# Kernel tuning notes

Measured on AMD Instinct MI355X. Metric: run time of the kernel, lower is better.

The kernel has to match this reference:

```python
import jax, jax.numpy as jnp
import numpy as np

NUM_HEADS = 4
HEAD_DIM = 64  # out_dim // num_heads
NEG_INF = -9e15


def setup_inputs() -> dict:
    key = jax.random.key(0)
    k1, k2, k3, k4 = jax.random.split(key, 4)
    b, n, in_dim, out_dim = 8, 1024, 256, 256
    x = jax.random.normal(k1, (b, n, in_dim), dtype=jnp.float32)
    adj = jax.random.uniform(k2, (b, n, n), dtype=jnp.float32)
    # linear_proj weight, stored as [in_dim, out_dim] (xavier-ish scale)
    Wp = jax.random.normal(k3, (in_dim, out_dim), dtype=jnp.float32) * (1.0 / np.sqrt(in_dim))
    # scoring_fn weight for concat([left(64), right(64), adj(1)]) -> 1
    Ws = jax.random.normal(k4, (2 * HEAD_DIM + 1,), dtype=jnp.float32) * (1.0 / np.sqrt(HEAD_DIM))
    bias = jnp.zeros((out_dim,), dtype=jnp.float32)
    return {"x": x, "adj": adj, "Wp": Wp, "Ws": Ws, "bias": bias}


def reference(x, adj, Wp, Ws, bias):
    b, n, _ = x.shape
    H, hd = NUM_HEADS, HEAD_DIM
    # manifold_in = Euclidean -> logmap0 is identity; dropout is eval (p=0)
    proj = (x @ Wp).reshape(b, n, H, hd)  # [b,n,H,hd]
    # scoring_fn(cat[left, right, adj]) decomposed: score = left.w_l + right.w_r + adj*w_a
    w_l, w_r, w_a = Ws[:hd], Ws[hd:2 * hd], Ws[2 * hd]
    s_l = jnp.einsum('bnhd,d->bnh', proj, w_l)  # dest-node term
    s_r = jnp.einsum('bmhd,d->bmh', proj, w_r)  # src-node term
    score = s_l[:, :, None, :] + s_r[:, None, :, :] + (adj * w_a)[..., None]  # [b,n,n,H]
    score = jax.nn.leaky_relu(score, 0.2)
    # local_agg: mask out non-edges (adj <= 1e-5) by adding -9e15
    pad = (adj <= 1e-5).astype(score.dtype)
    score = score + (NEG_INF * pad)[..., None]
    att = jax.nn.softmax(score, axis=2)  # softmax over source nodes m
    # msg[b,i,h,d] = sum_m att[b,i,m,h] * proj[b,m,h,d]
    msg = jnp.einsum('bimh,bmhd->bihd', att, proj).reshape(b, n, H * hd)
    # in_dim == out_dim -> no skip_proj; Euclidean expmap0/transp0/expmap: out = x + msg + bias
    out = x + msg + bias
    out = jax.nn.leaky_relu(out, 0.5)  # act = LeakyReLU(0.5)
    return out, adj
```

## Files before the change

kernel.cpp:

```cpp
#include <hip/hip_runtime.h>

#define NHEADS 4
#define HDIM   64
#define BATCH  8
#define SEQ    1024
#define CH     256
#define LOG2E  1.4426950408889634f
#define MC     128
#define NC     (SEQ / MC)
#define LDP    132

typedef float  f32x4  __attribute__((ext_vector_type(4)));
typedef __bf16 bf16x8 __attribute__((ext_vector_type(8)));
typedef short  s16x8  __attribute__((ext_vector_type(8)));
union FU { s16x8 s; bf16x8 b; };

__device__ inline unsigned short f2bf(float f) {
    unsigned u = __float_as_uint(f);
    return (unsigned short)((u + 0x7fffu + ((u >> 16) & 1u)) >> 16);
}
__device__ inline float4 nt_load4(const float* p) {
    f32x4 v = __builtin_nontemporal_load(reinterpret_cast<const f32x4*>(p));
    return make_float4(v.x, v.y, v.z, v.w);
}
__device__ inline void nt_store4(float* p, float4 v) {
    f32x4 u = {v.x, v.y, v.z, v.w};
    __builtin_nontemporal_store(u, reinterpret_cast<f32x4*>(p));
}


__global__ __launch_bounds__(256) void wpt_cast(const float* __restrict__ Wp,
                                                unsigned short* __restrict__ WpT) {
    __shared__ float T[32][33];
    const int t = threadIdx.x;
    const int kt = blockIdx.x * 32, ct = blockIdx.y * 32;
    const int r = t >> 3, c4 = (t & 7) * 4;
    float4 v = *reinterpret_cast<const float4*>(&Wp[(size_t)(kt + r) * CH + ct + c4]);
    T[r][c4 + 0] = v.x; T[r][c4 + 1] = v.y; T[r][c4 + 2] = v.z; T[r][c4 + 3] = v.w;
    __syncthreads();
    unsigned p0 = (unsigned)f2bf(T[c4 + 0][r]) | ((unsigned)f2bf(T[c4 + 1][r]) << 16);
    unsigned p1 = (unsigned)f2bf(T[c4 + 2][r]) | ((unsigned)f2bf(T[c4 + 3][r]) << 16);
    uint2 o = make_uint2(p0, p1);
    *reinterpret_cast<uint2*>(&WpT[(size_t)(ct + r) * CH + kt + c4]) = o;
}

__global__ __launch_bounds__(256, 2) void proj_fused(const float* __restrict__ x,
                                                     const unsigned short* __restrict__ WpT,
                                                     const float* __restrict__ Ws,
                                                     unsigned short* __restrict__ projT,
                                                     float* __restrict__ sl,
                                                     float* __restrict__ sr) {
    const int t = threadIdx.x, w = t >> 6, l = t & 63, il = l & 15, g = l >> 4;
    const int row0 = blockIdx.x * 16;
    const int b = row0 >> 10, n0 = row0 & 1023;

    const unsigned short* Ap = WpT + (size_t)(w * 64 + il) * CH + g * 8;
    const float*          Bp = x + (size_t)(row0 + il) * CH + g * 8;

    float4 xv[8][2];
#pragma unroll
    for (int kt = 0; kt < 8; ++kt) {
        xv[kt][0] = *reinterpret_cast<const float4*>(Bp + kt * 32);
        xv[kt][1] = *reinterpret_cast<const float4*>(Bp + kt * 32 + 4);
    }

    f32x4 acc[4] = {};
#pragma unroll
    for (int kt = 0; kt < 8; ++kt) {
        FU a[4], bb;
#pragma unroll
        for (int ai = 0; ai < 4; ++ai)
            a[ai].s = *reinterpret_cast<const s16x8*>(Ap + (size_t)ai * 16 * CH + kt * 32);
        bb.b[0] = (__bf16)xv[kt][0].x; bb.b[1] = (__bf16)xv[kt][0].y;
        bb.b[2] = (__bf16)xv[kt][0].z; bb.b[3] = (__bf16)xv[kt][0].w;
        bb.b[4] = (__bf16)xv[kt][1].x; bb.b[5] = (__bf16)xv[kt][1].y;
        bb.b[6] = (__bf16)xv[kt][1].z; bb.b[7] = (__bf16)xv[kt][1].w;
#pragma unroll
        for (int ai = 0; ai < 4; ++ai)
            acc[ai] = __builtin_amdgcn_mfma_f32_16x16x32_bf16(a[ai].b, bb.b, acc[ai], 0, 0, 0);
    }

    unsigned short* pS = projT + (((size_t)(b * NHEADS + w)) << 16)
                       + (size_t)(n0 >> 4) * 1024 + (il >> 3) * 128 + (il & 7);
#pragma unroll
    for (int ai = 0; ai < 4; ++ai)
#pragma unroll
        for (int q = 0; q < 4; ++q)
            pS[ai * 256 + (g * 4 + q) * 8] = f2bf(acc[ai][q]);

    float pl = 0.f, pr = 0.f;
#pragma unroll
    for (int ai = 0; ai < 4; ++ai) {
        float4 wlv = *reinterpret_cast<const float4*>(&Ws[ai * 16 + g * 4]);
        float4 wrv = *reinterpret_cast<const float4*>(&Ws[HDIM + ai * 16 + g * 4]);
        pl += acc[ai][0] * wlv.x + acc[ai][1] * wlv.y + acc[ai][2] * wlv.z + acc[ai][3] * wlv.w;
        pr += acc[ai][0] * wrv.x + acc[ai][1] * wrv.y + acc[ai][2] * wrv.z + acc[ai][3] * wrv.w;
    }
    pl += __shfl_xor(pl, 16); pl += __shfl_xor(pl, 32);
    pr += __shfl_xor(pr, 16); pr += __shfl_xor(pr, 32);
    if (l < 16) {
        sl[(size_t)(b * NHEADS + w) * SEQ + n0 + il] = pl * LOG2E;
        sr[(size_t)(b * NHEADS + w) * SEQ + n0 + il] = pr * LOG2E;
    }
}

template <bool FUSE_ADJ>
__global__ __launch_bounds__(256, 2) void attn12(const float* __restrict__ x,
                                                 const float* __restrict__ adj,
                                                 const unsigned short* __restrict__ projT,
                                                 const float* __restrict__ sl,
                                                 const float* __restrict__ sr,
                                                 const float* __restrict__ Ws,
                                                 const float* __restrict__ bias,
                                                 float* __restrict__ out,
                                                 float* __restrict__ out_adj) {
    __shared__ __align__(16) float abuf[2][16][LDP];

    const int t = threadIdx.x;
    const int h = t >> 6, l = t & 63, il = l & 15, g = l >> 4;
    const int b  = blockIdx.x & 7;
    const int i0 = (blockIdx.x >> 3) * 16;
    const float wa2 = Ws[2 * HDIM] * LOG2E;

    const int str = t >> 4;
    const int stc = (t & 15) * 4;
    const size_t astg = ((size_t)(b * SEQ + i0 + str)) * SEQ + stc;

    const float sl_i = sl[(size_t)(b * NHEADS + h) * SEQ + i0 + il];
    const float* srp = sr + (size_t)(b * NHEADS + h) * SEQ;
    const unsigned short* pTsw = projT + (((size_t)(b * NHEADS + h)) << 16)
                               + (g >> 1) * 1024 + (g & 1) * 128 + il * 8;

    FU ones;
#pragma unroll
    for (int j = 0; j < 8; ++j) ones.s[j] = (short)0x3F80;

    f32x4 acc[4] = {};
    f32x4 dacc = {};

    float4 c00 = nt_load4(adj + astg);
    float4 c01 = nt_load4(adj + astg + 64);
    float4 cur0 = nt_load4(adj + astg + MC);
    float4 cur1 = nt_load4(adj + astg + MC + 64);
    if (FUSE_ADJ) {
        nt_store4(out_adj + astg, c00);
        nt_store4(out_adj + astg + 64, c01);
    }
    *reinterpret_cast<float4*>(&abuf[0][str][stc])      = c00;
    *reinterpret_cast<float4*>(&abuf[0][str][stc + 64]) = c01;
    __syncthreads();

    for (int c = 0; c < NC; ++c) {
        float4 nx0 = {}, nx1 = {};
        if (c + 2 < NC) {
            nx0 = nt_load4(adj + astg + (size_t)(c + 2) * MC);
            nx1 = nt_load4(adj + astg + (size_t)(c + 2) * MC + 64);
        }
        const float* aT = &abuf[c & 1][il][0];
        const int mt = c * MC;

        float4 av[4][2], sv4[4][2];
        FU B[4][4];
#pragma unroll
        for (int kq = 0; kq < 4; ++kq) {
            const int mk = kq * 32 + g * 8;
            av[kq][0]  = *reinterpret_cast<const float4*>(aT + mk);
            av[kq][1]  = *reinterpret_cast<const float4*>(aT + mk + 4);
            sv4[kq][0] = *reinterpret_cast<const float4*>(srp + mt + mk);
            sv4[kq][1] = *reinterpret_cast<const float4*>(srp + mt + mk + 4);
        }
#pragma unroll
        for (int kq = 0; kq < 4; ++kq) {
#pragma unroll
            for (int bj = 0; bj < 4; ++bj)
                B[kq][bj].s = *reinterpret_cast<const s16x8*>(
                    pTsw + c * 8192 + kq * 2048 + bj * 256);
        }

        FU af[4];
#pragma unroll
        for (int kq = 0; kq < 4; ++kq) {
            float aj[8] = {av[kq][0].x, av[kq][0].y, av[kq][0].z, av[kq][0].w,
                           av[kq][1].x, av[kq][1].y, av[kq][1].z, av[kq][1].w};
            float sv[8] = {sv4[kq][0].x, sv4[kq][0].y, sv4[kq][0].z, sv4[kq][0].w,
                           sv4[kq][1].x, sv4[kq][1].y, sv4[kq][1].z, sv4[kq][1].w};
#pragma unroll
            for (int j = 0; j < 8; ++j) {
                float s = fmaf(aj[j], wa2, sl_i + sv[j]);
                s = __builtin_amdgcn_fmed3f(s, 0.2f * s, 86.5617f);
                float e = (aj[j] <= 1e-5f) ? 0.f : __builtin_amdgcn_exp2f(s);
                af[kq].b[j] = (__bf16)e;
            }
        }

#pragma unroll
        for (int kq = 0; kq < 4; ++kq) {
            acc[0] = __builtin_amdgcn_mfma_f32_16x16x32_bf16(af[kq].b, B[kq][0].b, acc[0], 0, 0, 0);
            acc[1] = __builtin_amdgcn_mfma_f32_16x16x32_bf16(af[kq].b, B[kq][1].b, acc[1], 0, 0, 0);
            acc[2] = __builtin_amdgcn_mfma_f32_16x16x32_bf16(af[kq].b, B[kq][2].b, acc[2], 0, 0, 0);
            acc[3] = __builtin_amdgcn_mfma_f32_16x16x32_bf16(af[kq].b, B[kq][3].b, acc[3], 0, 0, 0);
            dacc   = __builtin_amdgcn_mfma_f32_16x16x32_bf16(af[kq].b, ones.b,   dacc,   0, 0, 0);
        }

        if (c + 1 < NC) {
            if (FUSE_ADJ) {
                nt_store4(out_adj + astg + (size_t)(c + 1) * MC, cur0);
                nt_store4(out_adj + astg + (size_t)(c + 1) * MC + 64, cur1);
            }
            *reinterpret_cast<float4*>(&abuf[(c + 1) & 1][str][stc])      = cur0;
            *reinterpret_cast<float4*>(&abuf[(c + 1) & 1][str][stc + 64]) = cur1;
        }
        __syncthreads();
        cur0 = nx0; cur1 = nx1;
    }

    const float* bb = bias + h * HDIM;
#pragma unroll
    for (int q = 0; q < 4; ++q) {
        const float inv = 1.f / dacc[q];
        const size_t ob = ((size_t)(b * SEQ + i0 + g * 4 + q)) * CH + h * HDIM + il;
#pragma unroll
        for (int bj = 0; bj < 4; ++bj) {
            float v = fmaf(acc[bj][q], inv, x[ob + bj * 16] + bb[bj * 16 + il]);
            v = fmaxf(v, 0.5f * v);
            __builtin_nontemporal_store(v, out + ob + bj * 16);
        }
    }
}

__global__ void adjcopy(const float* __restrict__ adj, float* __restrict__ dst, int n4) {
    int idx = blockIdx.x * blockDim.x + threadIdx.x;
    int stride = gridDim.x * blockDim.x;
    const float4* s = reinterpret_cast<const float4*>(adj);
    float4* d = reinterpret_cast<float4*>(dst);
    for (int i = idx; i < n4; i += stride) d[i] = s[i];
}

extern "C" void kernel_launch(void* const* d_in, const int* in_sizes, int n_in,
                              void* d_out, int out_size, void* d_ws, size_t ws_size,
                              hipStream_t stream) {
    const float* x    = (const float*)d_in[0];
    const float* adj  = (const float*)d_in[1];
    const float* Wp   = (const float*)d_in[2];
    const float* Ws   = (const float*)d_in[3];
    const float* bias = (const float*)d_in[4];
    float* out     = (float*)d_out;
    float* out_adj = out + (size_t)BATCH * SEQ * CH;

    const size_t nProj = (size_t)BATCH * SEQ * CH;
    const size_t nSc   = (size_t)BATCH * NHEADS * SEQ;
    const size_t need  = CH * CH * 2 + nProj * 2 + 2 * nSc * 4;
    const bool use_ws  = (ws_size >= need);
    char* scratch = use_ws ? (char*)d_ws : (char*)out_adj;
    unsigned short* WpT   = (unsigned short*)scratch;
    unsigned short* projT = (unsigned short*)(scratch + (size_t)CH * CH * 2);
    float*          sl    = (float*)(scratch + (size_t)CH * CH * 2 + nProj * 2);
    float*          sr    = sl + nSc;

    wpt_cast<<<dim3(8, 8), 256, 0, stream>>>(Wp, WpT);
    proj_fused<<<dim3(512), 256, 0, stream>>>(x, WpT, Ws, projT, sl, sr);
    if (use_ws) {
        attn12<true><<<dim3(512), 256, 0, stream>>>(
            x, adj, projT, sl, sr, Ws, bias, out, out_adj);
    } else {
        attn12<false><<<dim3(512), 256, 0, stream>>>(
            x, adj, projT, sl, sr, Ws, bias, out, out_adj);
        adjcopy<<<2048, 256, 0, stream>>>(adj, out_adj, (BATCH * SEQ * SEQ) / 4);
    }
}
```

Baseline: 53.92 us.

## Split source-node range across two wave groups per block with LDS reduction

The attention kernel now runs 512 threads per block, with two groups of four waves that each handle half of the source-node range (512 columns), so each wave loops over 4 chunks instead of 8. Partial message accumulators and softmax denominators from the second half are written to shared memory, then summed by the first half before the epilogue. This shortens each wave's serial loop and raises the number of in-flight adj loads per block. In exchange it doubles shared memory for the adjacency staging, adds a block-wide reduction, and may reduce how many blocks fit per CU.

Result: faster. 51.26 us, median of 2 (-4.9%).

```diff
diff --git a/kernel.cpp b/kernel.cpp
--- a/kernel.cpp
+++ b/kernel.cpp
@@ -7,7 +7,6 @@
 #define CH     256
 #define LOG2E  1.4426950408889634f
 #define MC     128
-#define NC     (SEQ / MC)
 #define LDP    132
 
 typedef float  f32x4  __attribute__((ext_vector_type(4)));
@@ -105,7 +104,7 @@
 }
 
 template <bool FUSE_ADJ>
-__global__ __launch_bounds__(256, 2) void attn12(const float* __restrict__ x,
+__global__ __launch_bounds__(512, 2) void attn13(const float* __restrict__ x,
                                                  const float* __restrict__ adj,
                                                  const unsigned short* __restrict__ projT,
                                                  const float* __restrict__ sl,
@@ -114,21 +113,24 @@
                                                  const float* __restrict__ bias,
                                                  float* __restrict__ out,
                                                  float* __restrict__ out_adj) {
-    __shared__ __align__(16) float abuf[2][16][LDP];
+    __shared__ __align__(16) float abuf[2][2][16][LDP];
 
     const int t = threadIdx.x;
-    const int h = t >> 6, l = t & 63, il = l & 15, g = l >> 4;
+    const int w = t >> 6, l = t & 63, il = l & 15, g = l >> 4;
+    const int h = w & 3, mh = w >> 2;
     const int b  = blockIdx.x & 7;
     const int i0 = (blockIdx.x >> 3) * 16;
     const float wa2 = Ws[2 * HDIM] * LOG2E;
 
-    const int str = t >> 4;
+    const int sh = t >> 8;
+    const int str = (t >> 4) & 15;
     const int stc = (t & 15) * 4;
-    const size_t astg = ((size_t)(b * SEQ + i0 + str)) * SEQ + stc;
+    const size_t astg = ((size_t)(b * SEQ + i0 + str)) * SEQ + sh * 512 + stc;
 
     const float sl_i = sl[(size_t)(b * NHEADS + h) * SEQ + i0 + il];
-    const float* srp = sr + (size_t)(b * NHEADS + h) * SEQ;
+    const float* srp = sr + (size_t)(b * NHEADS + h) * SEQ + mh * 512;
     const unsigned short* pTsw = projT + (((size_t)(b * NHEADS + h)) << 16)
+                               + (size_t)mh * 32768
                                + (g >> 1) * 1024 + (g & 1) * 128 + il * 8;
 
     FU ones;
@@ -146,17 +148,17 @@
         nt_store4(out_adj + astg, c00);
         nt_store4(out_adj + astg + 64, c01);
     }
-    *reinterpret_cast<float4*>(&abuf[0][str][stc])      = c00;
-    *reinterpret_cast<float4*>(&abuf[0][str][stc + 64]) = c01;
+    *reinterpret_cast<float4*>(&abuf[0][sh][str][stc])      = c00;
+    *reinterpret_cast<float4*>(&abuf[0][sh][str][stc + 64]) = c01;
     __syncthreads();
 
-    for (int c = 0; c < NC; ++c) {
+    for (int c = 0; c < 4; ++c) {
         float4 nx0 = {}, nx1 = {};
-        if (c + 2 < NC) {
+        if (c + 2 < 4) {
             nx0 = nt_load4(adj + astg + (size_t)(c + 2) * MC);
             nx1 = nt_load4(adj + astg + (size_t)(c + 2) * MC + 64);
         }
-        const float* aT = &abuf[c & 1][il][0];
+        const float* aT = &abuf[c & 1][mh][il][0];
         const int mt = c * MC;
 
         float4 av[4][2], sv4[4][2];
@@ -202,28 +204,46 @@
             dacc   = __builtin_amdgcn_mfma_f32_16x16x32_bf16(af[kq].b, ones.b,   dacc,   0, 0, 0);
         }
 
-        if (c + 1 < NC) {
+        if (c + 1 < 4) {
             if (FUSE_ADJ) {
                 nt_store4(out_adj + astg + (size_t)(c + 1) * MC, cur0);
                 nt_store4(out_adj + astg + (size_t)(c + 1) * MC + 64, cur1);
             }
-            *reinterpret_cast<float4*>(&abuf[(c + 1) & 1][str][stc])      = cur0;
-            *reinterpret_cast<float4*>(&abuf[(c + 1) & 1][str][stc + 64]) = cur1;
+            *reinterpret_cast<float4*>(&abuf[(c + 1) & 1][sh][str][stc])      = cur0;
+            *reinterpret_cast<float4*>(&abuf[(c + 1) & 1][sh][str][stc + 64]) = cur1;
         }
         __syncthreads();
         cur0 = nx0; cur1 = nx1;
     }
 
-    const float* bb = bias + h * HDIM;
-#pragma unroll
-    for (int q = 0; q < 4; ++q) {
-        const float inv = 1.f / dacc[q];
-        const size_t ob = ((size_t)(b * SEQ + i0 + g * 4 + q)) * CH + h * HDIM + il;
-#pragma unroll
-        for (int bj = 0; bj < 4; ++bj) {
-            float v = fmaf(acc[bj][q], inv, x[ob + bj * 16] + bb[bj * 16 + il]);
-            v = fmaxf(v, 0.5f * v);
-            __builtin_nontemporal_store(v, out + ob + bj * 16);
+    float (*part)[16][68] = reinterpret_cast<float (*)[16][68]>(&abuf[0][0][0][0]);
+    if (mh == 1) {
+#pragma unroll
+        for (int bj = 0; bj < 4; ++bj)
+#pragma unroll
+            for (int q = 0; q < 4; ++q)
+                part[h][g * 4 + q][bj * 16 + il] = acc[bj][q];
+        if (il == 0) {
+#pragma unroll
+            for (int q = 0; q < 4; ++q) part[h][g * 4 + q][64] = dacc[q];
+        }
+    }
+    __syncthreads();
+    if (mh == 0) {
+        const float* bb = bias + h * HDIM;
+#pragma unroll
+        for (int q = 0; q < 4; ++q) {
+            const int row = g * 4 + q;
+            const float den = dacc[q] + part[h][row][64];
+            const float inv = 1.f / den;
+            const size_t ob = ((size_t)(b * SEQ + i0 + row)) * CH + h * HDIM + il;
+#pragma unroll
+            for (int bj = 0; bj < 4; ++bj) {
+                float m = acc[bj][q] + part[h][row][bj * 16 + il];
+                float v = fmaf(m, inv, x[ob + bj * 16] + bb[bj * 16 + il]);
+                v = fmaxf(v, 0.5f * v);
+                __builtin_nontemporal_store(v, out + ob + bj * 16);
+            }
         }
     }
 }
@@ -260,10 +280,10 @@
     wpt_cast<<<dim3(8, 8), 256, 0, stream>>>(Wp, WpT);
     proj_fused<<<dim3(512), 256, 0, stream>>>(x, WpT, Ws, projT, sl, sr);
     if (use_ws) {
-        attn12<true><<<dim3(512), 256, 0, stream>>>(
+        attn13<true><<<dim3(512), 512, 0, stream>>>(
             x, adj, projT, sl, sr, Ws, bias, out, out_adj);
     } else {
-        attn12<false><<<dim3(512), 256, 0, stream>>>(
+        attn13<false><<<dim3(512), 512, 0, stream>>>(
             x, adj, projT, sl, sr, Ws, bias, out, out_adj);
         adjcopy<<<2048, 256, 0, stream>>>(adj, out_adj, (BATCH * SEQ * SEQ) / 4);
     }
```

## Prefetch projT fragments one chunk ahead and stage sr scores in LDS

Applied to the files above, without the earlier changes.

The attention kernel now double-buffers the bf16 projT B fragments in registers, loading the next chunk's fragments while the current chunk's exponentials and MFMAs run. The per-head sr scores are copied once into shared memory instead of being re-read from global each chunk. The barrier becomes an inline asm waitcnt+s_barrier and the chunk loop is fully unrolled. These are meant to hide global load latency, at the cost of more VGPRs (two sets of 16 fragments), which risks spills or lower occupancy under launch_bounds(256,2), plus 16KB more LDS per block.

After: 52.93 us. About the same (-1.8%).

```diff
diff --git a/kernel.cpp b/kernel.cpp
--- a/kernel.cpp
+++ b/kernel.cpp
@@ -14,6 +14,8 @@
 typedef __bf16 bf16x8 __attribute__((ext_vector_type(8)));
 typedef short  s16x8  __attribute__((ext_vector_type(8)));
 union FU { s16x8 s; bf16x8 b; };
+
+#define BAR() asm volatile("s_waitcnt lgkmcnt(0)\n\ts_barrier" ::: "memory")
 
 __device__ inline unsigned short f2bf(float f) {
     unsigned u = __float_as_uint(f);
@@ -105,7 +107,7 @@
 }
 
 template <bool FUSE_ADJ>
-__global__ __launch_bounds__(256, 2) void attn12(const float* __restrict__ x,
+__global__ __launch_bounds__(256, 2) void attn14(const float* __restrict__ x,
                                                  const float* __restrict__ adj,
                                                  const unsigned short* __restrict__ projT,
                                                  const float* __restrict__ sl,
@@ -115,6 +117,7 @@
                                                  float* __restrict__ out,
                                                  float* __restrict__ out_adj) {
     __shared__ __align__(16) float abuf[2][16][LDP];
+    __shared__ __align__(16) float srl[NHEADS][SEQ];
 
     const int t = threadIdx.x;
     const int h = t >> 6, l = t & 63, il = l & 15, g = l >> 4;
@@ -127,7 +130,7 @@
     const size_t astg = ((size_t)(b * SEQ + i0 + str)) * SEQ + stc;
 
     const float sl_i = sl[(size_t)(b * NHEADS + h) * SEQ + i0 + il];
-    const float* srp = sr + (size_t)(b * NHEADS + h) * SEQ;
+    const float* srg = sr + (size_t)(b * NHEADS + h) * SEQ;
     const unsigned short* pTsw = projT + (((size_t)(b * NHEADS + h)) << 16)
                                + (g >> 1) * 1024 + (g & 1) * 128 + il * 8;
 
@@ -138,6 +141,11 @@
     f32x4 acc[4] = {};
     f32x4 dacc = {};
 
+#pragma unroll
+    for (int k = 0; k < 4; ++k) {
+        float4 sv = *reinterpret_cast<const float4*>(srg + l * 16 + k * 4);
+        *reinterpret_cast<float4*>(&srl[h][l * 16 + k * 4]) = sv;
+    }
     float4 c00 = nt_load4(adj + astg);
     float4 c01 = nt_load4(adj + astg + 64);
     float4 cur0 = nt_load4(adj + astg + MC);
@@ -148,35 +156,41 @@
     }
     *reinterpret_cast<float4*>(&abuf[0][str][stc])      = c00;
     *reinterpret_cast<float4*>(&abuf[0][str][stc + 64]) = c01;
+    FU Bb[2][4][4];
+#pragma unroll
+    for (int kq = 0; kq < 4; ++kq)
+#pragma unroll
+        for (int bj = 0; bj < 4; ++bj)
+            Bb[0][kq][bj].s = *reinterpret_cast<const s16x8*>(pTsw + kq * 2048 + bj * 256);
     __syncthreads();
 
+#pragma unroll
     for (int c = 0; c < NC; ++c) {
+        const int cb = c & 1, nb = cb ^ 1;
         float4 nx0 = {}, nx1 = {};
         if (c + 2 < NC) {
             nx0 = nt_load4(adj + astg + (size_t)(c + 2) * MC);
             nx1 = nt_load4(adj + astg + (size_t)(c + 2) * MC + 64);
         }
-        const float* aT = &abuf[c & 1][il][0];
-        const int mt = c * MC;
-
+        if (c + 1 < NC) {
+#pragma unroll
+            for (int kq = 0; kq < 4; ++kq)
+#pragma unroll
+                for (int bj = 0; bj < 4; ++bj)
+                    Bb[nb][kq][bj].s = *reinterpret_cast<const s16x8*>(
+                        pTsw + (c + 1) * 8192 + kq * 2048 + bj * 256);
+        }
+        const float* aT = &abuf[cb][il][0];
+        const float* sT = &srl[h][c * MC];
         float4 av[4][2], sv4[4][2];
-        FU B[4][4];
 #pragma unroll
         for (int kq = 0; kq < 4; ++kq) {
             const int mk = kq * 32 + g * 8;
             av[kq][0]  = *reinterpret_cast<const float4*>(aT + mk);
             av[kq][1]  = *reinterpret_cast<const float4*>(aT + mk + 4);
-            sv4[kq][0] = *reinterpret_cast<const float4*>(srp + mt + mk);
-            sv4[kq][1] = *reinterpret_cast<const float4*>(srp + mt + mk + 4);
-        }
-#pragma unroll
-        for (int kq = 0; kq < 4; ++kq) {
-#pragma unroll
-            for (int bj = 0; bj < 4; ++bj)
-                B[kq][bj].s = *reinterpret_cast<const s16x8*>(
-                    pTsw + c * 8192 + kq * 2048 + bj * 256);
-        }
-
+            sv4[kq][0] = *reinterpret_cast<const float4*>(sT + mk);
+            sv4[kq][1] = *reinterpret_cast<const float4*>(sT + mk + 4);
+        }
         FU af[4];
 #pragma unroll
         for (int kq = 0; kq < 4; ++kq) {
@@ -192,25 +206,23 @@
                 af[kq].b[j] = (__bf16)e;
             }
         }
-
 #pragma unroll
         for (int kq = 0; kq < 4; ++kq) {
-            acc[0] = __builtin_amdgcn_mfma_f32_16x16x32_bf16(af[kq].b, B[kq][0].b, acc[0], 0, 0, 0);
-            acc[1] = __builtin_amdgcn_mfma_f32_16x16x32_bf16(af[kq].b, B[kq][1].b, acc[1], 0, 0, 0);
-            acc[2] = __builtin_amdgcn_mfma_f32_16x16x32_bf16(af[kq].b, B[kq][2].b, acc[2], 0, 0, 0);
-            acc[3] = __builtin_amdgcn_mfma_f32_16x16x32_bf16(af[kq].b, B[kq][3].b, acc[3], 0, 0, 0);
-            dacc   = __builtin_amdgcn_mfma_f32_16x16x32_bf16(af[kq].b, ones.b,   dacc,   0, 0, 0);
-        }
-
+            acc[0] = __builtin_amdgcn_mfma_f32_16x16x32_bf16(af[kq].b, Bb[cb][kq][0].b, acc[0], 0, 0, 0);
+            acc[1] = __builtin_amdgcn_mfma_f32_16x16x32_bf16(af[kq].b, Bb[cb][kq][1].b, acc[1], 0, 0, 0);
+            acc[2] = __builtin_amdgcn_mfma_f32_16x16x32_bf16(af[kq].b, Bb[cb][kq][2].b, acc[2], 0, 0, 0);
+            acc[3] = __builtin_amdgcn_mfma_f32_16x16x32_bf16(af[kq].b, Bb[cb][kq][3].b, acc[3], 0, 0, 0);
+            dacc   = __builtin_amdgcn_mfma_f32_16x16x32_bf16(af[kq].b, ones.b,          dacc,   0, 0, 0);
+        }
         if (c + 1 < NC) {
             if (FUSE_ADJ) {
                 nt_store4(out_adj + astg + (size_t)(c + 1) * MC, cur0);
                 nt_store4(out_adj + astg + (size_t)(c + 1) * MC + 64, cur1);
             }
-            *reinterpret_cast<float4*>(&abuf[(c + 1) & 1][str][stc])      = cur0;
-            *reinterpret_cast<float4*>(&abuf[(c + 1) & 1][str][stc + 64]) = cur1;
-        }
-        __syncthreads();
+            *reinterpret_cast<float4*>(&abuf[nb][str][stc])      = cur0;
+            *reinterpret_cast<float4*>(&abuf[nb][str][stc + 64]) = cur1;
+        }
+        BAR();
         cur0 = nx0; cur1 = nx1;
     }
 
@@ -260,10 +272,10 @@
     wpt_cast<<<dim3(8, 8), 256, 0, stream>>>(Wp, WpT);
     proj_fused<<<dim3(512), 256, 0, stream>>>(x, WpT, Ws, projT, sl, sr);
     if (use_ws) {
-        attn12<true><<<dim3(512), 256, 0, stream>>>(
+        attn14<true><<<dim3(512), 256, 0, stream>>>(
             x, adj, projT, sl, sr, Ws, bias, out, out_adj);
     } else {
-        attn12<false><<<dim3(512), 256, 0, stream>>>(
+        attn14<false><<<dim3(512), 256, 0, stream>>>(
             x, adj, projT, sl, sr, Ws, bias, out, out_adj);
         adjcopy<<<2048, 256, 0, stream>>>(adj, out_adj, (BATCH * SEQ * SEQ) / 4);
     }
```
